# Optimization experiments

Measured on AMD Instinct MI355X. Metric: run time of the kernel, lower is better.

The kernel has to match this reference:

```python
import jax, jax.numpy as jnp
import numpy as np

B, S, H = 1, 2048, 1024
NH, NKV, D = 16, 4, 64
E, TOPK, F = 8, 2, 1024
EPS = 1e-5
ALPHA = 1.702
LIMIT = 7.0
THETA = 10000.0


def setup_inputs() -> dict:
    key = jax.random.key(0)
    ks = jax.random.split(key, 16)
    rn = lambda k, shape, s=0.02: (jax.random.normal(k, shape, jnp.float32) * s)
    qkv_out = (NH + 2 * NKV) * D
    return {
        "hidden_states": jax.random.normal(ks[0], (B, S, H), jnp.float32),
        "residual": jax.random.normal(ks[1], (B, S, H), jnp.float32),
        "positions": jnp.broadcast_to(jnp.arange(S, dtype=jnp.int32), (B, S)),
        "ln1_w": jnp.ones((H,), jnp.float32),
        "ln2_w": jnp.ones((H,), jnp.float32),
        "qkv_w": rn(ks[2], (qkv_out, H)),
        "qkv_b": rn(ks[3], (qkv_out,)),
        "sinks": rn(ks[4], (NH,), 1.0),
        "o_w": rn(ks[5], (H, NH * D)),
        "o_b": rn(ks[6], (H,)),
        "router_w": rn(ks[7], (E, H)),
        "router_b": rn(ks[8], (E,)),
        "gate_up_w": rn(ks[9], (E, 2 * F, H)),
        "gate_up_b": rn(ks[10], (E, 2 * F)),
        "down_w": rn(ks[11], (E, H, F)),
        "down_b": rn(ks[12], (E, H)),
    }


def _rmsnorm(x, w):
    return x * jax.lax.rsqrt(jnp.mean(x * x, -1, keepdims=True) + EPS) * w


def _rope(x, pos):
    # x: [B, S, Hn, D]; pos: [B, S]
    half = D // 2
    inv_freq = 1.0 / (THETA ** (jnp.arange(half, dtype=jnp.float32) / half))
    ang = pos.astype(jnp.float32)[..., None] * inv_freq            # [B,S,half]
    cos = jnp.concatenate([jnp.cos(ang)] * 2, -1)[:, :, None, :]    # [B,S,1,D]
    sin = jnp.concatenate([jnp.sin(ang)] * 2, -1)[:, :, None, :]
    x1, x2 = x[..., :half], x[..., half:]
    rot = jnp.concatenate([-x2, x1], -1)
    return x * cos + rot * sin


def reference(hidden_states, residual, positions, ln1_w, ln2_w, qkv_w, qkv_b,
              sinks, o_w, o_b, router_w, router_b, gate_up_w, gate_up_b,
              down_w, down_b):
    # --- fused RMSNorm + residual (pre-attn) ---
    res1 = hidden_states + residual
    h = _rmsnorm(res1, ln1_w)

    # --- attention ---
    qkv = h @ qkv_w.T + qkv_b
    q, k, v = jnp.split(qkv, [NH * D, NH * D + NKV * D], axis=-1)
    Q = _rope(q.reshape(B, S, NH, D), positions).transpose(0, 2, 1, 3)   # [B,NH,S,D]
    K = _rope(k.reshape(B, S, NKV, D), positions).transpose(0, 2, 1, 3)  # [B,NKV,S,D]
    V = v.reshape(B, S, NKV, D).transpose(0, 2, 1, 3)
    g = NH // NKV
    K = jnp.repeat(K, g, axis=1)
    V = jnp.repeat(V, g, axis=1)
    scores = jnp.einsum('bhqd,bhkd->bhqk', Q, K) * (D ** -0.5)
    causal = jnp.tril(jnp.ones((S, S), bool))
    scores = jnp.where(causal, scores, -1e30)
    sink = jnp.broadcast_to(sinks[None, :, None, None], (B, NH, S, 1))
    probs = jax.nn.softmax(jnp.concatenate([scores, sink], -1), axis=-1)[..., :S]
    attn = jnp.einsum('bhqk,bhkd->bhqd', probs, V)
    attn = attn.transpose(0, 2, 1, 3).reshape(B, S, NH * D)
    attn = attn @ o_w.T + o_b

    # --- fused RMSNorm + residual (post-attn) ---
    res2 = attn + res1
    h2 = _rmsnorm(res2, ln2_w)

    # --- MoE: top-k router + gated expert MLPs ---
    x = h2.reshape(-1, H)                                  # [T,H]
    logits = x @ router_w.T + router_b                      # [T,E]
    vals, idx = jax.lax.top_k(logits, TOPK)
    w = jax.nn.softmax(vals, axis=-1)
    T = B * S
    rscores = jnp.zeros_like(logits).at[jnp.arange(T)[:, None], idx].set(w)  # [T,E]
    gu = jnp.einsum('th,efh->tef', x, gate_up_w) + gate_up_b  # [T,E,2F]
    gate = jnp.minimum(gu[..., 0::2], LIMIT)
    up = jnp.clip(gu[..., 1::2], -LIMIT, LIMIT)
    glu = gate * jax.nn.sigmoid(gate * ALPHA)
    act = (up + 1.0) * glu                                   # [T,E,F]
    eout = jnp.einsum('tef,ehf->teh', act, down_w) + down_b   # [T,E,H]
    moe = jnp.einsum('teh,te->th', eout, rscores).reshape(B, S, H)
    return moe, res2
```

## Files before the change

### kernel.cpp

```cpp
#include <hip/hip_runtime.h>
#include <math.h>

constexpr int S_ = 2048, H_ = 1024, NH_ = 16, NKV_ = 4, D_ = 64;
constexpr int QKV_ = (NH_ + 2 * NKV_) * D_;
constexpr int E_ = 8, F_ = 1024;
constexpr float EPS_ = 1e-5f, ALPHA_ = 1.702f, LIMIT_ = 7.0f;

typedef __attribute__((ext_vector_type(8))) short short8;
typedef __attribute__((ext_vector_type(4))) float f32x4;

__device__ __forceinline__ short f2bf(float f) {
  union { float f; unsigned u; } v; v.f = f;
  unsigned r = v.u + 0x7fffu + ((v.u >> 16) & 1u);
  return (short)(r >> 16);
}

__device__ __forceinline__ void gload_lds16(const void* g, void* l) {
  __builtin_amdgcn_global_load_lds((const __attribute__((address_space(1))) void*)g,
                                   (__attribute__((address_space(3))) void*)l, 16, 0, 0);
}

__global__ __launch_bounds__(256) void k_cvt(const float* __restrict__ in,
                                             short* __restrict__ out, int n4) {
  int i = blockIdx.x * 256 + threadIdx.x;
  int stride = gridDim.x * 256;
  for (; i < n4; i += stride) {
    float4 v = ((const float4*)in)[i];
    short4 o;
    o.x = f2bf(v.x); o.y = f2bf(v.y); o.z = f2bf(v.z); o.w = f2bf(v.w);
    ((short4*)out)[i] = o;
  }
}

__global__ __launch_bounds__(256) void k_norm(const float* __restrict__ x,
                                              const float* __restrict__ add,
                                              const float* __restrict__ w,
                                              float* __restrict__ sum_out,
                                              float* __restrict__ nrm_out,
                                              short* __restrict__ nrm_bf) {
  int t = blockIdx.x, tid = threadIdx.x;
  int lane = tid & 63, wid = tid >> 6;
  float v[4];
  float ss = 0.f;
#pragma unroll
  for (int i = 0; i < 4; i++) {
    int c = i * 256 + tid;
    float a = x[(size_t)t * H_ + c];
    if (add) a += add[(size_t)t * H_ + c];
    v[i] = a;
    ss += a * a;
  }
#pragma unroll
  for (int off = 32; off > 0; off >>= 1) ss += __shfl_xor(ss, off);
  __shared__ float red[4];
  __shared__ float scsh;
  if (lane == 0) red[wid] = ss;
  __syncthreads();
  if (tid == 0) scsh = rsqrtf((red[0] + red[1] + red[2] + red[3]) * (1.f / H_) + EPS_);
  __syncthreads();
  float sc = scsh;
#pragma unroll
  for (int i = 0; i < 4; i++) {
    int c = i * 256 + tid;
    float nv = v[i] * sc * w[c];
    if (sum_out) sum_out[(size_t)t * H_ + c] = v[i];
    if (nrm_out) nrm_out[(size_t)t * H_ + c] = nv;
    if (nrm_bf)  nrm_bf[(size_t)t * H_ + c] = f2bf(nv);
  }
}

__device__ __forceinline__ void mfma_core(const short* __restrict__ A, int lda,
                                          const short* __restrict__ B, int ldb,
                                          int n0, int K,
                                          const int* rows_sh, char* smem,
                                          f32x4 acc[4][4]) {
  const int tid = threadIdx.x;
  const int wid = tid >> 6, lane = tid & 63;
  const int wr = wid >> 1, wc = wid & 1;
  const int fl = lane & 15, fh = lane >> 4;
  const short* src[4];
  unsigned lofs[4];
  {
    const int kofs = (lane & 3) * 8;
    const int r4 = lane >> 2;
#pragma unroll
    for (int j = 0; j < 4; j++) {
      int inst = (wid & 1) * 4 + j;
      int row = inst * 16 + r4;
      if (wid < 2) {
        src[j] = A + (size_t)rows_sh[row] * lda + kofs;
        lofs[j] = inst * 1024u;
      } else {
        src[j] = B + (size_t)(n0 + row) * ldb + kofs;
        lofs[j] = 8192u + inst * 1024u;
      }
    }
  }
  char* As = smem;
  char* Bs = smem + 8192;
  const int abase = (wr * 64 + fl) * 64 + fh * 16;
  const int bbase = (wc * 64 + fl) * 64 + fh * 16;
  for (int kt = 0; kt < K; kt += 32) {
#pragma unroll
    for (int j = 0; j < 4; j++) gload_lds16(src[j] + kt, smem + lofs[j]);
    asm volatile("s_waitcnt vmcnt(0)" ::: "memory");
    __syncthreads();
    short8 a[4], b[4];
#pragma unroll
    for (int mi = 0; mi < 4; mi++) a[mi] = *(const short8*)(As + abase + mi * 1024);
#pragma unroll
    for (int nj = 0; nj < 4; nj++) b[nj] = *(const short8*)(Bs + bbase + nj * 1024);
#pragma unroll
    for (int mi = 0; mi < 4; mi++)
#pragma unroll
      for (int nj = 0; nj < 4; nj++)
        acc[mi][nj] = __builtin_amdgcn_mfma_f32_16x16x32_bf16(a[mi], b[nj], acc[mi][nj], 0, 0, 0);
    __syncthreads();
  }
}

__global__ __launch_bounds__(256) void k_mfma_qkv(const short* __restrict__ A,
                                                  const short* __restrict__ W,
                                                  const float* __restrict__ bias,
                                                  float* __restrict__ out) {
  __shared__ __align__(16) char smem[16384];
  __shared__ int rows_sh[128];
  int m0 = blockIdx.y * 128, n0 = blockIdx.x * 128;
  int tid = threadIdx.x;
  if (tid < 128) rows_sh[tid] = m0 + tid;
  __syncthreads();
  f32x4 acc[4][4] = {};
  mfma_core(A, H_, W, H_, n0, H_, rows_sh, smem, acc);
  const int wid = tid >> 6, lane = tid & 63;
  const int wr = wid >> 1, wc = wid & 1, fl = lane & 15, fh = lane >> 4;
#pragma unroll
  for (int mi = 0; mi < 4; mi++)
#pragma unroll
    for (int nj = 0; nj < 4; nj++) {
      int c = n0 + wc * 64 + nj * 16 + fl;
      float bv = bias[c];
#pragma unroll
      for (int j = 0; j < 4; j++) {
        int r = m0 + wr * 64 + mi * 16 + fh * 4 + j;
        out[(size_t)r * QKV_ + c] = acc[mi][nj][j] + bv;
      }
    }
}

__global__ __launch_bounds__(256) void k_mfma_o(const short* __restrict__ A,
                                                const short* __restrict__ W,
                                                const float* __restrict__ bias,
                                                const float* __restrict__ res1,
                                                float* __restrict__ res2) {
  __shared__ __align__(16) char smem[16384];
  __shared__ int rows_sh[128];
  int m0 = blockIdx.y * 128, n0 = blockIdx.x * 128;
  int tid = threadIdx.x;
  if (tid < 128) rows_sh[tid] = m0 + tid;
  __syncthreads();
  f32x4 acc[4][4] = {};
  mfma_core(A, H_, W, H_, n0, H_, rows_sh, smem, acc);
  const int wid = tid >> 6, lane = tid & 63;
  const int wr = wid >> 1, wc = wid & 1, fl = lane & 15, fh = lane >> 4;
#pragma unroll
  for (int mi = 0; mi < 4; mi++)
#pragma unroll
    for (int nj = 0; nj < 4; nj++) {
      int c = n0 + wc * 64 + nj * 16 + fl;
      float bv = bias[c];
#pragma unroll
      for (int j = 0; j < 4; j++) {
        int r = m0 + wr * 64 + mi * 16 + fh * 4 + j;
        res2[(size_t)r * H_ + c] = acc[mi][nj][j] + bv + res1[(size_t)r * H_ + c];
      }
    }
}

__global__ void k_rope_cvt(const float* __restrict__ qkv, const int* __restrict__ positions,
                           short* __restrict__ qb, short* __restrict__ kb) {
  int idx = blockIdx.x * 256 + threadIdx.x;
  int i = idx & 31;
  int hd = (idx >> 5) % 20;
  int t = idx / (20 * 32);
  const float* base = qkv + (size_t)t * QKV_ + (hd < NH_ ? hd * D_ : NH_ * D_ + (hd - NH_) * D_);
  float pos = (float)positions[t];
  float invf = powf(10000.f, -(float)i * (1.f / 32.f));
  float ang = pos * invf;
  float sn, cs;
  sincosf(ang, &sn, &cs);
  float x1 = base[i], x2 = base[i + 32];
  float r1 = x1 * cs - x2 * sn;
  float r2 = x2 * cs + x1 * sn;
  if (hd < NH_) {
    short* o = qb + (size_t)t * H_ + hd * D_;
    o[i]      = f2bf(r1 * 0.125f);
    o[i + 32] = f2bf(r2 * 0.125f);
  } else {
    short* o = kb + (size_t)t * (NKV_ * D_) + (hd - NH_) * D_;
    o[i]      = f2bf(r1);
    o[i + 32] = f2bf(r2);
  }
}

__global__ __launch_bounds__(256) void k_vcvt(const float* __restrict__ qkv,
                                              short* __restrict__ vbT) {
  int id = blockIdx.x * 256 + threadIdx.x;
  int t = id & (S_ - 1);
  int rest = id >> 11;
  int d = rest & 63;
  int kvh = rest >> 6;
  vbT[id] = f2bf(qkv[(size_t)t * QKV_ + (NH_ + NKV_) * D_ + kvh * D_ + d]);
}

__global__ __launch_bounds__(256) void k_attn_mfma(const short* __restrict__ qb,
                                                   const short* __restrict__ kb,
                                                   const short* __restrict__ vbT,
                                                   const float* __restrict__ sinks,
                                                   short* __restrict__ attnb) {
  const int h = blockIdx.y;
  const int kvh = h >> 2;
  const int tid = threadIdx.x;
  const int wid = tid >> 6, lane = tid & 63;
  const int fl = lane & 15, fh = lane >> 4;

  __shared__ __align__(16) short Ks[64 * 64];
  __shared__ __align__(16) short Vts[64 * 64];
  __shared__ short Pl[4][16][72];

  const float snk = sinks[h];
  const int srcoff = 8 * ((lane & 7) ^ (lane >> 3));
  const int srow = lane >> 3;

#pragma unroll
  for (int rep = 0; rep < 2; rep++) {
    const int qt = rep == 0 ? blockIdx.x : 31 - blockIdx.x;
    const int qbase = qt * 64;
    const int qrow = qbase + wid * 16 + fl;
    short8 qa[2];
#pragma unroll
    for (int p = 0; p < 2; p++)
      qa[p] = *(const short8*)(qb + (size_t)qrow * H_ + h * 64 + p * 32 + fh * 8);

    float mreg[4], lreg[4];
    f32x4 oacc[4] = {};
#pragma unroll
    for (int j = 0; j < 4; j++) { mreg[j] = -1e30f; lreg[j] = 0.f; }

    for (int kc = 0; kc <= qt; kc++) {
#pragma unroll
      for (int ii = 0; ii < 2; ii++) {
        int inst = wid * 2 + ii;
        int krow = kc * 64 + inst * 8 + srow;
        gload_lds16(kb + (size_t)krow * (NKV_ * D_) + kvh * D_ + srcoff,
                    (char*)Ks + inst * 1024);
        int drow = inst * 8 + srow;
        gload_lds16(vbT + (size_t)(kvh * 64 + drow) * S_ + kc * 64 + srcoff,
                    (char*)Vts + inst * 1024);
      }
      asm volatile("s_waitcnt vmcnt(0)" ::: "memory");
      __syncthreads();

      f32x4 sacc[4] = {};
#pragma unroll
      for (int p = 0; p < 2; p++) {
        const int cswz_base = (p * 4 + fh);
#pragma unroll
        for (int t = 0; t < 4; t++) {
          int r = t * 16 + fl;
          short8 kf = *(const short8*)((const char*)Ks + r * 128 + 16 * (cswz_base ^ (fl & 7)));
          sacc[t] = __builtin_amdgcn_mfma_f32_16x16x32_bf16(qa[p], kf, sacc[t], 0, 0, 0);
        }
      }
      if (kc == qt) {
#pragma unroll
        for (int t = 0; t < 4; t++) {
          int key = kc * 64 + t * 16 + fl;
#pragma unroll
          for (int j = 0; j < 4; j++) {
            int q = qbase + wid * 16 + fh * 4 + j;
            if (key > q) sacc[t][j] = -1e30f;
          }
        }
      }
#pragma unroll
      for (int j = 0; j < 4; j++) {
        float vm = fmaxf(fmaxf(sacc[0][j], sacc[1][j]), fmaxf(sacc[2][j], sacc[3][j]));
        vm = fmaxf(vm, __shfl_xor(vm, 1));
        vm = fmaxf(vm, __shfl_xor(vm, 2));
        vm = fmaxf(vm, __shfl_xor(vm, 4));
        vm = fmaxf(vm, __shfl_xor(vm, 8));
        float mn = fmaxf(mreg[j], vm);
        float sf = __expf(mreg[j] - mn);
        float ps = 0.f;
#pragma unroll
        for (int t = 0; t < 4; t++) {
          float pv = __expf(sacc[t][j] - mn);
          ps += pv;
          Pl[wid][fh * 4 + j][t * 16 + fl] = f2bf(pv);
        }
        ps += __shfl_xor(ps, 1);
        ps += __shfl_xor(ps, 2);
        ps += __shfl_xor(ps, 4);
        ps += __shfl_xor(ps, 8);
        lreg[j] = lreg[j] * sf + ps;
        mreg[j] = mn;
#pragma unroll
        for (int u = 0; u < 4; u++) oacc[u][j] *= sf;
      }
#pragma unroll
      for (int p = 0; p < 2; p++) {
        short8 pa = *(const short8*)((const char*)&Pl[wid][0][0] + fl * 144 + p * 64 + fh * 16);
        const int cswz_base = (p * 4 + fh);
#pragma unroll
        for (int u = 0; u < 4; u++) {
          int r = u * 16 + fl;
          short8 vf = *(const short8*)((const char*)Vts + r * 128 + 16 * (cswz_base ^ (fl & 7)));
          oacc[u] = __builtin_amdgcn_mfma_f32_16x16x32_bf16(pa, vf, oacc[u], 0, 0, 0);
        }
      }
      __syncthreads();
    }
#pragma unroll
    for (int j = 0; j < 4; j++) {
      float mf = fmaxf(mreg[j], snk);
      float denom = lreg[j] * __expf(mreg[j] - mf) + __expf(snk - mf);
      float osc = __expf(mreg[j] - mf) / denom;
      int q = qbase + wid * 16 + fh * 4 + j;
#pragma unroll
      for (int u = 0; u < 4; u++)
        attnb[(size_t)q * H_ + h * 64 + u * 16 + fl] = f2bf(oacc[u][j] * osc);
    }
  }
}

__global__ __launch_bounds__(64) void k_router(const float* __restrict__ h2,
                                               const float* __restrict__ rw,
                                               const float* __restrict__ rb,
                                               int* __restrict__ counts,
                                               int* __restrict__ perm,
                                               float* __restrict__ pw) {
  int t = blockIdx.x, lane = threadIdx.x;
  float acc[E_];
#pragma unroll
  for (int e = 0; e < E_; e++) acc[e] = 0.f;
  for (int i = 0; i < 16; i++) {
    float x = h2[(size_t)t * H_ + i * 64 + lane];
#pragma unroll
    for (int e = 0; e < E_; e++) acc[e] += x * rw[e * H_ + i * 64 + lane];
  }
#pragma unroll
  for (int e = 0; e < E_; e++) {
#pragma unroll
    for (int off = 32; off > 0; off >>= 1) acc[e] += __shfl_xor(acc[e], off);
  }
  if (lane == 0) {
    float lg[E_];
#pragma unroll
    for (int e = 0; e < E_; e++) lg[e] = acc[e] + rb[e];
    int i0 = 0;
    float v0 = lg[0];
    for (int e = 1; e < E_; e++)
      if (lg[e] > v0) { v0 = lg[e]; i0 = e; }
    int i1 = -1;
    float v1 = -INFINITY;
    for (int e = 0; e < E_; e++) {
      if (e == i0) continue;
      if (lg[e] > v1) { v1 = lg[e]; i1 = e; }
    }
    float ex = expf(v1 - v0);
    float w0 = 1.f / (1.f + ex);
    float w1 = ex * w0;
    int p0 = atomicAdd(&counts[i0], 1);
    if (p0 < S_) { perm[i0 * S_ + p0] = t * 2;     pw[i0 * S_ + p0] = w0; }
    int p1 = atomicAdd(&counts[i1], 1);
    if (p1 < S_) { perm[i1 * S_ + p1] = t * 2 + 1; pw[i1 * S_ + p1] = w1; }
  }
}

__global__ __launch_bounds__(256) void k_mfma_gu(const short* __restrict__ h2b,
                                                 const short* __restrict__ W,
                                                 const float* __restrict__ gu_b,
                                                 const int* __restrict__ counts,
                                                 const int* __restrict__ perm,
                                                 short* __restrict__ actb) {
  int e = blockIdx.z;
  int cnt = counts[e];
  if (cnt < 0) cnt = 0;
  if (cnt > S_) cnt = S_;
  int m0 = blockIdx.y * 128;
  if (m0 >= cnt) return;
  int n0 = blockIdx.x * 128;
  __shared__ __align__(16) char smem[16384];
  __shared__ int rows_sh[128];
  __shared__ int slots_sh[128];
  int tid = threadIdx.x;
  if (tid < 128) {
    int idx = m0 + tid;
    int p = (idx < cnt) ? perm[e * S_ + idx] : -1;
    if (p < 0 || p >= 2 * S_) p = -1;
    slots_sh[tid] = p;
    rows_sh[tid] = (p >= 0) ? (p >> 1) : 0;
  }
  __syncthreads();
  f32x4 acc[4][4] = {};
  mfma_core(h2b, H_, W + (size_t)e * 2 * F_ * H_, H_, n0, H_, rows_sh, smem, acc);
  const int wid = tid >> 6, lane = tid & 63;
  const int wr = wid >> 1, wc = wid & 1, fl = lane & 15, fh = lane >> 4;
  const float* gub = gu_b + (size_t)e * 2 * F_;
#pragma unroll
  for (int mi = 0; mi < 4; mi++)
#pragma unroll
    for (int nj = 0; nj < 4; nj++) {
      int c = n0 + wc * 64 + nj * 16 + fl;
      float bv = gub[c];
#pragma unroll
      for (int j = 0; j < 4; j++) {
        int r = wr * 64 + mi * 16 + fh * 4 + j;
        float v = acc[mi][nj][j] + bv;
        float other = __shfl_xor(v, 1);
        if (!(lane & 1)) {
          int slot = slots_sh[r];
          if (slot >= 0) {
            float g = fminf(v, LIMIT_);
            float u = fminf(fmaxf(other, -LIMIT_), LIMIT_);
            float a = (u + 1.f) * (g / (1.f + expf(-g * ALPHA_)));
            actb[(size_t)slot * F_ + (c >> 1)] = f2bf(a);
          }
        }
      }
    }
}

__global__ __launch_bounds__(256) void k_mfma_down(const short* __restrict__ actb,
                                                   const short* __restrict__ W,
                                                   const float* __restrict__ dn_b,
                                                   const int* __restrict__ counts,
                                                   const int* __restrict__ perm,
                                                   const float* __restrict__ pw,
                                                   float* __restrict__ dnout) {
  int e = blockIdx.z;
  int cnt = counts[e];
  if (cnt < 0) cnt = 0;
  if (cnt > S_) cnt = S_;
  int m0 = blockIdx.y * 128;
  if (m0 >= cnt) return;
  int n0 = blockIdx.x * 128;
  __shared__ __align__(16) char smem[16384];
  __shared__ int rows_sh[128];
  __shared__ float wts_sh[128];
  int tid = threadIdx.x;
  if (tid < 128) {
    int idx = m0 + tid;
    int p = 0;
    float w = 0.f;
    if (idx < cnt) { p = perm[e * S_ + idx]; w = pw[e * S_ + idx]; }
    if (p < 0 || p >= 2 * S_) { p = 0; w = 0.f; }
    rows_sh[tid] = p;
    wts_sh[tid] = w;
  }
  __syncthreads();
  f32x4 acc[4][4] = {};
  mfma_core(actb, F_, rows_sh == nullptr ? actb : (W + (size_t)e * H_ * F_), F_, n0, F_, rows_sh, smem, acc);
  const int wid = tid >> 6, lane = tid & 63;
  const int wr = wid >> 1, wc = wid & 1, fl = lane & 15, fh = lane >> 4;
  const float* dnb = dn_b + (size_t)e * H_;
#pragma unroll
  for (int mi = 0; mi < 4; mi++)
#pragma unroll
    for (int nj = 0; nj < 4; nj++) {
      int c = n0 + wc * 64 + nj * 16 + fl;
      float bv = dnb[c];
#pragma unroll
      for (int j = 0; j < 4; j++) {
        int r = wr * 64 + mi * 16 + fh * 4 + j;
        if (m0 + r < cnt) {
          int slot = rows_sh[r];
          dnout[(size_t)slot * H_ + c] = (acc[mi][nj][j] + bv) * wts_sh[r];
        }
      }
    }
}

__global__ __launch_bounds__(256) void k_combine(const float* __restrict__ dnout,
                                                 float* __restrict__ out) {
  int i = blockIdx.x * 256 + threadIdx.x;
  int t = i >> 8, c = i & 255;
  const float4* a = (const float4*)dnout;
  float4 x = a[(size_t)(2 * t) * 256 + c];
  float4 y = a[(size_t)(2 * t + 1) * 256 + c];
  float4 o;
  o.x = x.x + y.x; o.y = x.y + y.y; o.z = x.z + y.z; o.w = x.w + y.w;
  ((float4*)out)[i] = o;
}

extern "C" void kernel_launch(void* const* d_in, const int* in_sizes, int n_in,
                              void* d_out, int out_size, void* d_ws, size_t ws_size,
                              hipStream_t stream) {
  (void)in_sizes; (void)n_in; (void)out_size; (void)ws_size;
  const float* hidden   = (const float*)d_in[0];
  const float* residual = (const float*)d_in[1];
  const int*   positions= (const int*)d_in[2];
  const float* ln1_w    = (const float*)d_in[3];
  const float* ln2_w    = (const float*)d_in[4];
  const float* qkv_w    = (const float*)d_in[5];
  const float* qkv_b    = (const float*)d_in[6];
  const float* sinks    = (const float*)d_in[7];
  const float* o_w      = (const float*)d_in[8];
  const float* o_b      = (const float*)d_in[9];
  const float* router_w = (const float*)d_in[10];
  const float* router_b = (const float*)d_in[11];
  const float* gu_w     = (const float*)d_in[12];
  const float* gu_b     = (const float*)d_in[13];
  const float* dn_w     = (const float*)d_in[14];
  const float* dn_b     = (const float*)d_in[15];

  float* out_moe = (float*)d_out;
  float* res2 = (float*)d_out + (size_t)S_ * H_;

  char* ws = (char*)d_ws;
  size_t off = 0;
  auto alloc = [&](size_t bytes) {
    void* p = ws + off;
    off = (off + bytes + 255) & ~(size_t)255;
    return p;
  };
  int*   counts  = (int*)alloc(E_ * sizeof(int));
  int*   perm    = (int*)alloc((size_t)E_ * S_ * sizeof(int));
  float* pw      = (float*)alloc((size_t)E_ * S_ * sizeof(float));
  float* res1    = (float*)alloc((size_t)S_ * H_ * 4);
  short* hbuf_b  = (short*)alloc((size_t)S_ * H_ * 2);
  float* qkv     = (float*)alloc((size_t)S_ * QKV_ * 4);
  short* qb      = (short*)alloc((size_t)S_ * H_ * 2);
  short* kb      = (short*)alloc((size_t)S_ * NKV_ * D_ * 2);
  short* vbT     = (short*)alloc((size_t)S_ * NKV_ * D_ * 2);
  short* attnb   = (short*)alloc((size_t)S_ * H_ * 2);
  float* h2      = (float*)alloc((size_t)S_ * H_ * 4);
  short* h2b     = (short*)alloc((size_t)S_ * H_ * 2);
  short* actb    = (short*)alloc((size_t)2 * S_ * F_ * 2);
  float* dnout   = (float*)alloc((size_t)2 * S_ * H_ * 4);
  short* qkv_wb  = (short*)alloc((size_t)QKV_ * H_ * 2);
  short* o_wb    = (short*)alloc((size_t)H_ * H_ * 2);
  short* gu_wb   = (short*)alloc((size_t)E_ * 2 * F_ * H_ * 2);
  short* dn_wb   = (short*)alloc((size_t)E_ * H_ * F_ * 2);

  hipMemsetAsync(counts, 0, E_ * sizeof(int), stream);

  k_cvt<<<1024, 256, 0, stream>>>(qkv_w, qkv_wb, QKV_ * H_ / 4);
  k_cvt<<<1024, 256, 0, stream>>>(o_w, o_wb, H_ * H_ / 4);
  k_cvt<<<2048, 256, 0, stream>>>(gu_w, gu_wb, E_ * 2 * F_ * H_ / 4);
  k_cvt<<<2048, 256, 0, stream>>>(dn_w, dn_wb, E_ * H_ * F_ / 4);

  k_norm<<<S_, 256, 0, stream>>>(hidden, residual, ln1_w, res1, nullptr, hbuf_b);
  k_mfma_qkv<<<dim3(QKV_ / 128, S_ / 128), 256, 0, stream>>>(hbuf_b, qkv_wb, qkv_b, qkv);
  k_rope_cvt<<<(S_ * 20 * 32) / 256, 256, 0, stream>>>(qkv, positions, qb, kb);
  k_vcvt<<<(S_ * NKV_ * D_) / 256, 256, 0, stream>>>(qkv, vbT);
  k_attn_mfma<<<dim3(16, NH_), 256, 0, stream>>>(qb, kb, vbT, sinks, attnb);
  k_mfma_o<<<dim3(H_ / 128, S_ / 128), 256, 0, stream>>>(attnb, o_wb, o_b, res1, res2);
  k_norm<<<S_, 256, 0, stream>>>(res2, nullptr, ln2_w, nullptr, h2, h2b);
  k_router<<<S_, 64, 0, stream>>>(h2, router_w, router_b, counts, perm, pw);
  k_mfma_gu<<<dim3(2 * F_ / 128, S_ / 128, E_), 256, 0, stream>>>(h2b, gu_wb, gu_b, counts, perm, actb);
  k_mfma_down<<<dim3(H_ / 128, S_ / 128, E_), 256, 0, stream>>>(actb, dn_wb, dn_b, counts, perm, pw, dnout);
  k_combine<<<(S_ * H_ / 4) / 256, 256, 0, stream>>>(dnout, out_moe);
}
```

Measured before the change: 451.3 us.

## Double-buffer GEMM and attention loads, fuse router into norm, atomic MoE combine

```diff
diff --git a/kernel.cpp b/kernel.cpp
--- a/kernel.cpp
+++ b/kernel.cpp
@@ -36,8 +36,12 @@
                                               const float* __restrict__ add,
                                               const float* __restrict__ w,
                                               float* __restrict__ sum_out,
-                                              float* __restrict__ nrm_out,
-                                              short* __restrict__ nrm_bf) {
+                                              short* __restrict__ nrm_bf,
+                                              const float* __restrict__ rw,
+                                              const float* __restrict__ rb,
+                                              int* __restrict__ counts,
+                                              int* __restrict__ perm,
+                                              float* __restrict__ pw) {
   int t = blockIdx.x, tid = threadIdx.x;
   int lane = tid & 63, wid = tid >> 6;
   float v[4];
@@ -59,13 +63,58 @@
   if (tid == 0) scsh = rsqrtf((red[0] + red[1] + red[2] + red[3]) * (1.f / H_) + EPS_);
   __syncthreads();
   float sc = scsh;
+  float nv[4];
 #pragma unroll
   for (int i = 0; i < 4; i++) {
     int c = i * 256 + tid;
-    float nv = v[i] * sc * w[c];
+    nv[i] = v[i] * sc * w[c];
     if (sum_out) sum_out[(size_t)t * H_ + c] = v[i];
-    if (nrm_out) nrm_out[(size_t)t * H_ + c] = nv;
-    if (nrm_bf)  nrm_bf[(size_t)t * H_ + c] = f2bf(nv);
+    nrm_bf[(size_t)t * H_ + c] = f2bf(nv[i]);
+  }
+  if (rw) {
+    float acc[E_];
+#pragma unroll
+    for (int e = 0; e < E_; e++) acc[e] = 0.f;
+#pragma unroll
+    for (int i = 0; i < 4; i++) {
+      int c = i * 256 + tid;
+#pragma unroll
+      for (int e = 0; e < E_; e++) acc[e] += nv[i] * rw[e * H_ + c];
+    }
+#pragma unroll
+    for (int e = 0; e < E_; e++) {
+#pragma unroll
+      for (int off = 32; off > 0; off >>= 1) acc[e] += __shfl_xor(acc[e], off);
+    }
+    __shared__ float rsh[4][E_];
+    if (lane == 0) {
+#pragma unroll
+      for (int e = 0; e < E_; e++) rsh[wid][e] = acc[e];
+    }
+    __syncthreads();
+    if (tid == 0) {
+      float lg[E_];
+#pragma unroll
+      for (int e = 0; e < E_; e++)
+        lg[e] = rsh[0][e] + rsh[1][e] + rsh[2][e] + rsh[3][e] + rb[e];
+      int i0 = 0;
+      float v0 = lg[0];
+      for (int e = 1; e < E_; e++)
+        if (lg[e] > v0) { v0 = lg[e]; i0 = e; }
+      int i1 = -1;
+      float v1 = -INFINITY;
+      for (int e = 0; e < E_; e++) {
+        if (e == i0) continue;
+        if (lg[e] > v1) { v1 = lg[e]; i1 = e; }
+      }
+      float ex = __expf(v1 - v0);
+      float w0 = 1.f / (1.f + ex);
+      float w1 = ex * w0;
+      int p0 = atomicAdd(&counts[i0], 1);
+      if (p0 < S_) { perm[i0 * S_ + p0] = t * 2;     pw[i0 * S_ + p0] = w0; }
+      int p1 = atomicAdd(&counts[i1], 1);
+      if (p1 < S_) { perm[i1 * S_ + p1] = t * 2 + 1; pw[i1 * S_ + p1] = w1; }
+    }
   }
 }
 
@@ -96,15 +145,25 @@
       }
     }
   }
-  char* As = smem;
-  char* Bs = smem + 8192;
   const int abase = (wr * 64 + fl) * 64 + fh * 16;
   const int bbase = (wc * 64 + fl) * 64 + fh * 16;
-  for (int kt = 0; kt < K; kt += 32) {
-#pragma unroll
-    for (int j = 0; j < 4; j++) gload_lds16(src[j] + kt, smem + lofs[j]);
-    asm volatile("s_waitcnt vmcnt(0)" ::: "memory");
+  const int T = K >> 5;
+#pragma unroll
+  for (int j = 0; j < 4; j++) gload_lds16(src[j], smem + lofs[j]);
+  int cur = 0;
+  for (int t = 0; t < T; t++) {
+    if (t + 1 < T) {
+      int kt = (t + 1) << 5;
+#pragma unroll
+      for (int j = 0; j < 4; j++)
+        gload_lds16(src[j] + kt, smem + ((cur ^ 1) * 16384u + lofs[j]));
+      asm volatile("s_waitcnt vmcnt(4)" ::: "memory");
+    } else {
+      asm volatile("s_waitcnt vmcnt(0)" ::: "memory");
+    }
     __syncthreads();
+    const char* As = smem + cur * 16384u;
+    const char* Bs = As + 8192;
     short8 a[4], b[4];
 #pragma unroll
     for (int mi = 0; mi < 4; mi++) a[mi] = *(const short8*)(As + abase + mi * 1024);
@@ -116,6 +175,7 @@
       for (int nj = 0; nj < 4; nj++)
         acc[mi][nj] = __builtin_amdgcn_mfma_f32_16x16x32_bf16(a[mi], b[nj], acc[mi][nj], 0, 0, 0);
     __syncthreads();
+    cur ^= 1;
   }
 }
 
@@ -123,7 +183,7 @@
                                                   const short* __restrict__ W,
                                                   const float* __restrict__ bias,
                                                   float* __restrict__ out) {
-  __shared__ __align__(16) char smem[16384];
+  __shared__ __align__(16) char smem[32768];
   __shared__ int rows_sh[128];
   int m0 = blockIdx.y * 128, n0 = blockIdx.x * 128;
   int tid = threadIdx.x;
@@ -152,7 +212,7 @@
                                                 const float* __restrict__ bias,
                                                 const float* __restrict__ res1,
                                                 float* __restrict__ res2) {
-  __shared__ __align__(16) char smem[16384];
+  __shared__ __align__(16) char smem[32768];
   __shared__ int rows_sh[128];
   int m0 = blockIdx.y * 128, n0 = blockIdx.x * 128;
   int tid = threadIdx.x;
@@ -184,10 +244,9 @@
   int t = idx / (20 * 32);
   const float* base = qkv + (size_t)t * QKV_ + (hd < NH_ ? hd * D_ : NH_ * D_ + (hd - NH_) * D_);
   float pos = (float)positions[t];
-  float invf = powf(10000.f, -(float)i * (1.f / 32.f));
+  float invf = exp2f(-(float)i * 0.4152410118609203f);
   float ang = pos * invf;
-  float sn, cs;
-  sincosf(ang, &sn, &cs);
+  float sn = __sinf(ang), cs = __cosf(ang);
   float x1 = base[i], x2 = base[i + 32];
   float r1 = x1 * cs - x2 * sn;
   float r2 = x2 * cs + x1 * sn;
@@ -202,14 +261,24 @@
   }
 }
 
-__global__ __launch_bounds__(256) void k_vcvt(const float* __restrict__ qkv,
-                                              short* __restrict__ vbT) {
-  int id = blockIdx.x * 256 + threadIdx.x;
-  int t = id & (S_ - 1);
-  int rest = id >> 11;
-  int d = rest & 63;
-  int kvh = rest >> 6;
-  vbT[id] = f2bf(qkv[(size_t)t * QKV_ + (NH_ + NKV_) * D_ + kvh * D_ + d]);
+__global__ __launch_bounds__(256) void k_vtrans(const float* __restrict__ qkv,
+                                                short* __restrict__ vbT) {
+  __shared__ short tile[64][65];
+  int t0 = blockIdx.x * 64;
+  int kvh = blockIdx.y;
+  int tid = threadIdx.x;
+  int r = tid >> 6, c = tid & 63;
+#pragma unroll
+  for (int i = 0; i < 16; i++) {
+    int row = i * 4 + r;
+    tile[row][c] = f2bf(qkv[(size_t)(t0 + row) * QKV_ + (NH_ + NKV_) * D_ + kvh * D_ + c]);
+  }
+  __syncthreads();
+#pragma unroll
+  for (int i = 0; i < 16; i++) {
+    int d = i * 4 + r;
+    vbT[(size_t)(kvh * 64 + d) * S_ + t0 + c] = tile[c][d];
+  }
 }
 
 __global__ __launch_bounds__(256) void k_attn_mfma(const short* __restrict__ qb,
@@ -219,161 +288,127 @@
                                                    short* __restrict__ attnb) {
   const int h = blockIdx.y;
   const int kvh = h >> 2;
+  const int qt = (h < 8) ? blockIdx.x : 31 - blockIdx.x;
   const int tid = threadIdx.x;
   const int wid = tid >> 6, lane = tid & 63;
   const int fl = lane & 15, fh = lane >> 4;
 
-  __shared__ __align__(16) short Ks[64 * 64];
-  __shared__ __align__(16) short Vts[64 * 64];
+  __shared__ __align__(16) short Ks[2][4096];
+  __shared__ __align__(16) short Vts[2][4096];
   __shared__ short Pl[4][16][72];
 
   const float snk = sinks[h];
   const int srcoff = 8 * ((lane & 7) ^ (lane >> 3));
   const int srow = lane >> 3;
 
-#pragma unroll
-  for (int rep = 0; rep < 2; rep++) {
-    const int qt = rep == 0 ? blockIdx.x : 31 - blockIdx.x;
-    const int qbase = qt * 64;
-    const int qrow = qbase + wid * 16 + fl;
-    short8 qa[2];
-#pragma unroll
-    for (int p = 0; p < 2; p++)
-      qa[p] = *(const short8*)(qb + (size_t)qrow * H_ + h * 64 + p * 32 + fh * 8);
-
-    float mreg[4], lreg[4];
-    f32x4 oacc[4] = {};
-#pragma unroll
-    for (int j = 0; j < 4; j++) { mreg[j] = -1e30f; lreg[j] = 0.f; }
-
-    for (int kc = 0; kc <= qt; kc++) {
+  const int qbase = qt * 64;
+  const int qrow = qbase + wid * 16 + fl;
+  short8 qa[2];
+#pragma unroll
+  for (int p = 0; p < 2; p++)
+    qa[p] = *(const short8*)(qb + (size_t)qrow * H_ + h * 64 + p * 32 + fh * 8);
+
+  float mreg[4], lreg[4];
+  f32x4 oacc[4] = {};
+#pragma unroll
+  for (int j = 0; j < 4; j++) { mreg[j] = -1e30f; lreg[j] = 0.f; }
+
+#pragma unroll
+  for (int ii = 0; ii < 2; ii++) {
+    int inst = wid * 2 + ii;
+    gload_lds16(kb + (size_t)(inst * 8 + srow) * (NKV_ * D_) + kvh * D_ + srcoff,
+                (char*)Ks[0] + inst * 1024);
+    gload_lds16(vbT + (size_t)(kvh * 64 + inst * 8 + srow) * S_ + srcoff,
+                (char*)Vts[0] + inst * 1024);
+  }
+  int cur = 0;
+  for (int kc = 0; kc <= qt; kc++) {
+    if (kc < qt) {
+      int kn = kc + 1;
 #pragma unroll
       for (int ii = 0; ii < 2; ii++) {
         int inst = wid * 2 + ii;
-        int krow = kc * 64 + inst * 8 + srow;
-        gload_lds16(kb + (size_t)krow * (NKV_ * D_) + kvh * D_ + srcoff,
-                    (char*)Ks + inst * 1024);
-        int drow = inst * 8 + srow;
-        gload_lds16(vbT + (size_t)(kvh * 64 + drow) * S_ + kc * 64 + srcoff,
-                    (char*)Vts + inst * 1024);
-      }
+        gload_lds16(kb + (size_t)(kn * 64 + inst * 8 + srow) * (NKV_ * D_) + kvh * D_ + srcoff,
+                    (char*)Ks[cur ^ 1] + inst * 1024);
+        gload_lds16(vbT + (size_t)(kvh * 64 + inst * 8 + srow) * S_ + kn * 64 + srcoff,
+                    (char*)Vts[cur ^ 1] + inst * 1024);
+      }
+      asm volatile("s_waitcnt vmcnt(4)" ::: "memory");
+    } else {
       asm volatile("s_waitcnt vmcnt(0)" ::: "memory");
-      __syncthreads();
-
-      f32x4 sacc[4] = {};
-#pragma unroll
-      for (int p = 0; p < 2; p++) {
-        const int cswz_base = (p * 4 + fh);
-#pragma unroll
-        for (int t = 0; t < 4; t++) {
-          int r = t * 16 + fl;
-          short8 kf = *(const short8*)((const char*)Ks + r * 128 + 16 * (cswz_base ^ (fl & 7)));
-          sacc[t] = __builtin_amdgcn_mfma_f32_16x16x32_bf16(qa[p], kf, sacc[t], 0, 0, 0);
+    }
+    __syncthreads();
+
+    f32x4 sacc[4] = {};
+#pragma unroll
+    for (int p = 0; p < 2; p++) {
+      const int cswz_base = (p * 4 + fh);
+#pragma unroll
+      for (int t = 0; t < 4; t++) {
+        int r = t * 16 + fl;
+        short8 kf = *(const short8*)((const char*)Ks[cur] + r * 128 + 16 * (cswz_base ^ (fl & 7)));
+        sacc[t] = __builtin_amdgcn_mfma_f32_16x16x32_bf16(qa[p], kf, sacc[t], 0, 0, 0);
+      }
+    }
+    if (kc == qt) {
+#pragma unroll
+      for (int t = 0; t < 4; t++) {
+        int key = kc * 64 + t * 16 + fl;
+#pragma unroll
+        for (int j = 0; j < 4; j++) {
+          int q = qbase + wid * 16 + fh * 4 + j;
+          if (key > q) sacc[t][j] = -1e30f;
         }
       }
-      if (kc == qt) {
-#pragma unroll
-        for (int t = 0; t < 4; t++) {
-          int key = kc * 64 + t * 16 + fl;
-#pragma unroll
-          for (int j = 0; j < 4; j++) {
-            int q = qbase + wid * 16 + fh * 4 + j;
-            if (key > q) sacc[t][j] = -1e30f;
-          }
-        }
-      }
-#pragma unroll
-      for (int j = 0; j < 4; j++) {
-        float vm = fmaxf(fmaxf(sacc[0][j], sacc[1][j]), fmaxf(sacc[2][j], sacc[3][j]));
-        vm = fmaxf(vm, __shfl_xor(vm, 1));
-        vm = fmaxf(vm, __shfl_xor(vm, 2));
-        vm = fmaxf(vm, __shfl_xor(vm, 4));
-        vm = fmaxf(vm, __shfl_xor(vm, 8));
-        float mn = fmaxf(mreg[j], vm);
-        float sf = __expf(mreg[j] - mn);
-        float ps = 0.f;
-#pragma unroll
-        for (int t = 0; t < 4; t++) {
-          float pv = __expf(sacc[t][j] - mn);
-          ps += pv;
-          Pl[wid][fh * 4 + j][t * 16 + fl] = f2bf(pv);
-        }
-        ps += __shfl_xor(ps, 1);
-        ps += __shfl_xor(ps, 2);
-        ps += __shfl_xor(ps, 4);
-        ps += __shfl_xor(ps, 8);
-        lreg[j] = lreg[j] * sf + ps;
-        mreg[j] = mn;
-#pragma unroll
-        for (int u = 0; u < 4; u++) oacc[u][j] *= sf;
-      }
-#pragma unroll
-      for (int p = 0; p < 2; p++) {
-        short8 pa = *(const short8*)((const char*)&Pl[wid][0][0] + fl * 144 + p * 64 + fh * 16);
-        const int cswz_base = (p * 4 + fh);
-#pragma unroll
-        for (int u = 0; u < 4; u++) {
-          int r = u * 16 + fl;
-          short8 vf = *(const short8*)((const char*)Vts + r * 128 + 16 * (cswz_base ^ (fl & 7)));
-          oacc[u] = __builtin_amdgcn_mfma_f32_16x16x32_bf16(pa, vf, oacc[u], 0, 0, 0);
-        }
-      }
-      __syncthreads();
     }
 #pragma unroll
     for (int j = 0; j < 4; j++) {
-      float mf = fmaxf(mreg[j], snk);
-      float denom = lreg[j] * __expf(mreg[j] - mf) + __expf(snk - mf);
-      float osc = __expf(mreg[j] - mf) / denom;
-      int q = qbase + wid * 16 + fh * 4 + j;
-#pragma unroll
-      for (int u = 0; u < 4; u++)
-        attnb[(size_t)q * H_ + h * 64 + u * 16 + fl] = f2bf(oacc[u][j] * osc);
-    }
-  }
-}
-
-__global__ __launch_bounds__(64) void k_router(const float* __restrict__ h2,
-                                               const float* __restrict__ rw,
-                                               const float* __restrict__ rb,
-                                               int* __restrict__ counts,
-                                               int* __restrict__ perm,
-                                               float* __restrict__ pw) {
-  int t = blockIdx.x, lane = threadIdx.x;
-  float acc[E_];
-#pragma unroll
-  for (int e = 0; e < E_; e++) acc[e] = 0.f;
-  for (int i = 0; i < 16; i++) {
-    float x = h2[(size_t)t * H_ + i * 64 + lane];
-#pragma unroll
-    for (int e = 0; e < E_; e++) acc[e] += x * rw[e * H_ + i * 64 + lane];
-  }
-#pragma unroll
-  for (int e = 0; e < E_; e++) {
-#pragma unroll
-    for (int off = 32; off > 0; off >>= 1) acc[e] += __shfl_xor(acc[e], off);
-  }
-  if (lane == 0) {
-    float lg[E_];
-#pragma unroll
-    for (int e = 0; e < E_; e++) lg[e] = acc[e] + rb[e];
-    int i0 = 0;
-    float v0 = lg[0];
-    for (int e = 1; e < E_; e++)
-      if (lg[e] > v0) { v0 = lg[e]; i0 = e; }
-    int i1 = -1;
-    float v1 = -INFINITY;
-    for (int e = 0; e < E_; e++) {
-      if (e == i0) continue;
-      if (lg[e] > v1) { v1 = lg[e]; i1 = e; }
-    }
-    float ex = expf(v1 - v0);
-    float w0 = 1.f / (1.f + ex);
-    float w1 = ex * w0;
-    int p0 = atomicAdd(&counts[i0], 1);
-    if (p0 < S_) { perm[i0 * S_ + p0] = t * 2;     pw[i0 * S_ + p0] = w0; }
-    int p1 = atomicAdd(&counts[i1], 1);
-    if (p1 < S_) { perm[i1 * S_ + p1] = t * 2 + 1; pw[i1 * S_ + p1] = w1; }
+      float vm = fmaxf(fmaxf(sacc[0][j], sacc[1][j]), fmaxf(sacc[2][j], sacc[3][j]));
+      vm = fmaxf(vm, __shfl_xor(vm, 1));
+      vm = fmaxf(vm, __shfl_xor(vm, 2));
+      vm = fmaxf(vm, __shfl_xor(vm, 4));
+      vm = fmaxf(vm, __shfl_xor(vm, 8));
+      float mn = fmaxf(mreg[j], vm);
+      float sf = __expf(mreg[j] - mn);
+      float ps = 0.f;
+#pragma unroll
+      for (int t = 0; t < 4; t++) {
+        float pv = __expf(sacc[t][j] - mn);
+        ps += pv;
+        Pl[wid][fh * 4 + j][t * 16 + fl] = f2bf(pv);
+      }
+      ps += __shfl_xor(ps, 1);
+      ps += __shfl_xor(ps, 2);
+      ps += __shfl_xor(ps, 4);
+      ps += __shfl_xor(ps, 8);
+      lreg[j] = lreg[j] * sf + ps;
+      mreg[j] = mn;
+#pragma unroll
+      for (int u = 0; u < 4; u++) oacc[u][j] *= sf;
+    }
+#pragma unroll
+    for (int p = 0; p < 2; p++) {
+      short8 pa = *(const short8*)((const char*)&Pl[wid][0][0] + fl * 144 + p * 64 + fh * 16);
+      const int cswz_base = (p * 4 + fh);
+#pragma unroll
+      for (int u = 0; u < 4; u++) {
+        int r = u * 16 + fl;
+        short8 vf = *(const short8*)((const char*)Vts[cur] + r * 128 + 16 * (cswz_base ^ (fl & 7)));
+        oacc[u] = __builtin_amdgcn_mfma_f32_16x16x32_bf16(pa, vf, oacc[u], 0, 0, 0);
+      }
+    }
+    __syncthreads();
+    cur ^= 1;
+  }
+#pragma unroll
+  for (int j = 0; j < 4; j++) {
+    float mf = fmaxf(mreg[j], snk);
+    float denom = lreg[j] * __expf(mreg[j] - mf) + __expf(snk - mf);
+    float osc = __expf(mreg[j] - mf) / denom;
+    int q = qbase + wid * 16 + fh * 4 + j;
+#pragma unroll
+    for (int u = 0; u < 4; u++)
+      attnb[(size_t)q * H_ + h * 64 + u * 16 + fl] = f2bf(oacc[u][j] * osc);
   }
 }
 
@@ -390,7 +425,7 @@
   int m0 = blockIdx.y * 128;
   if (m0 >= cnt) return;
   int n0 = blockIdx.x * 128;
-  __shared__ __align__(16) char smem[16384];
+  __shared__ __align__(16) char smem[32768];
   __shared__ int rows_sh[128];
   __shared__ int slots_sh[128];
   int tid = threadIdx.x;
@@ -423,7 +458,7 @@
           if (slot >= 0) {
             float g = fminf(v, LIMIT_);
             float u = fminf(fmaxf(other, -LIMIT_), LIMIT_);
-            float a = (u + 1.f) * (g / (1.f + expf(-g * ALPHA_)));
+            float a = (u + 1.f) * (g / (1.f + __expf(-g * ALPHA_)));
             actb[(size_t)slot * F_ + (c >> 1)] = f2bf(a);
           }
         }
@@ -437,7 +472,7 @@
                                                    const int* __restrict__ counts,
                                                    const int* __restrict__ perm,
                                                    const float* __restrict__ pw,
-                                                   float* __restrict__ dnout) {
+                                                   float* __restrict__ out_moe) {
   int e = blockIdx.z;
   int cnt = counts[e];
   if (cnt < 0) cnt = 0;
@@ -445,7 +480,7 @@
   int m0 = blockIdx.y * 128;
   if (m0 >= cnt) return;
   int n0 = blockIdx.x * 128;
-  __shared__ __align__(16) char smem[16384];
+  __shared__ __align__(16) char smem[32768];
   __shared__ int rows_sh[128];
   __shared__ float wts_sh[128];
   int tid = threadIdx.x;
@@ -460,7 +495,7 @@
   }
   __syncthreads();
   f32x4 acc[4][4] = {};
-  mfma_core(actb, F_, rows_sh == nullptr ? actb : (W + (size_t)e * H_ * F_), F_, n0, F_, rows_sh, smem, acc);
+  mfma_core(actb, F_, W + (size_t)e * H_ * F_, F_, n0, F_, rows_sh, smem, acc);
   const int wid = tid >> 6, lane = tid & 63;
   const int wr = wid >> 1, wc = wid & 1, fl = lane & 15, fh = lane >> 4;
   const float* dnb = dn_b + (size_t)e * H_;
@@ -475,22 +510,11 @@
         int r = wr * 64 + mi * 16 + fh * 4 + j;
         if (m0 + r < cnt) {
           int slot = rows_sh[r];
-          dnout[(size_t)slot * H_ + c] = (acc[mi][nj][j] + bv) * wts_sh[r];
+          float val = (acc[mi][nj][j] + bv) * wts_sh[r];
+          atomicAdd(&out_moe[(size_t)(slot >> 1) * H_ + c], val);
         }
       }
     }
-}
-
-__global__ __launch_bounds__(256) void k_combine(const float* __restrict__ dnout,
-                                                 float* __restrict__ out) {
-  int i = blockIdx.x * 256 + threadIdx.x;
-  int t = i >> 8, c = i & 255;
-  const float4* a = (const float4*)dnout;
-  float4 x = a[(size_t)(2 * t) * 256 + c];
-  float4 y = a[(size_t)(2 * t + 1) * 256 + c];
-  float4 o;
-  o.x = x.x + y.x; o.y = x.y + y.y; o.z = x.z + y.z; o.w = x.w + y.w;
-  ((float4*)out)[i] = o;
 }
 
 extern "C" void kernel_launch(void* const* d_in, const int* in_sizes, int n_in,
@@ -534,31 +558,30 @@
   short* kb      = (short*)alloc((size_t)S_ * NKV_ * D_ * 2);
   short* vbT     = (short*)alloc((size_t)S_ * NKV_ * D_ * 2);
   short* attnb   = (short*)alloc((size_t)S_ * H_ * 2);
-  float* h2      = (float*)alloc((size_t)S_ * H_ * 4);
   short* h2b     = (short*)alloc((size_t)S_ * H_ * 2);
   short* actb    = (short*)alloc((size_t)2 * S_ * F_ * 2);
-  float* dnout   = (float*)alloc((size_t)2 * S_ * H_ * 4);
   short* qkv_wb  = (short*)alloc((size_t)QKV_ * H_ * 2);
   short* o_wb    = (short*)alloc((size_t)H_ * H_ * 2);
   short* gu_wb   = (short*)alloc((size_t)E_ * 2 * F_ * H_ * 2);
   short* dn_wb   = (short*)alloc((size_t)E_ * H_ * F_ * 2);
 
   hipMemsetAsync(counts, 0, E_ * sizeof(int), stream);
+  hipMemsetAsync(out_moe, 0, (size_t)S_ * H_ * 4, stream);
 
   k_cvt<<<1024, 256, 0, stream>>>(qkv_w, qkv_wb, QKV_ * H_ / 4);
   k_cvt<<<1024, 256, 0, stream>>>(o_w, o_wb, H_ * H_ / 4);
   k_cvt<<<2048, 256, 0, stream>>>(gu_w, gu_wb, E_ * 2 * F_ * H_ / 4);
   k_cvt<<<2048, 256, 0, stream>>>(dn_w, dn_wb, E_ * H_ * F_ / 4);
 
-  k_norm<<<S_, 256, 0, stream>>>(hidden, residual, ln1_w, res1, nullptr, hbuf_b);
+  k_norm<<<S_, 256, 0, stream>>>(hidden, residual, ln1_w, res1, hbuf_b,
+                                 nullptr, nullptr, nullptr, nullptr, nullptr);
   k_mfma_qkv<<<dim3(QKV_ / 128, S_ / 128), 256, 0, stream>>>(hbuf_b, qkv_wb, qkv_b, qkv);
   k_rope_cvt<<<(S_ * 20 * 32) / 256, 256, 0, stream>>>(qkv, positions, qb, kb);
-  k_vcvt<<<(S_ * NKV_ * D_) / 256, 256, 0, stream>>>(qkv, vbT);
-  k_attn_mfma<<<dim3(16, NH_), 256, 0, stream>>>(qb, kb, vbT, sinks, attnb);
+  k_vtrans<<<dim3(S_ / 64, NKV_), 256, 0, stream>>>(qkv, vbT);
+  k_attn_mfma<<<dim3(32, NH_), 256, 0, stream>>>(qb, kb, vbT, sinks, attnb);
   k_mfma_o<<<dim3(H_ / 128, S_ / 128), 256, 0, stream>>>(attnb, o_wb, o_b, res1, res2);
-  k_norm<<<S_, 256, 0, stream>>>(res2, nullptr, ln2_w, nullptr, h2, h2b);
-  k_router<<<S_, 64, 0, stream>>>(h2, router_w, router_b, counts, perm, pw);
+  k_norm<<<S_, 256, 0, stream>>>(res2, nullptr, ln2_w, nullptr, h2b,
+                                 router_w, router_b, counts, perm, pw);
   k_mfma_gu<<<dim3(2 * F_ / 128, S_ / 128, E_), 256, 0, stream>>>(h2b, gu_wb, gu_b, counts, perm, actb);
-  k_mfma_down<<<dim3(H_ / 128, S_ / 128, E_), 256, 0, stream>>>(actb, dn_wb, dn_b, counts, perm, pw, dnout);
-  k_combine<<<(S_ * H_ / 4) / 256, 256, 0, stream>>>(dnout, out_moe);
-}
+  k_mfma_down<<<dim3(H_ / 128, S_ / 128, E_), 256, 0, stream>>>(actb, dn_wb, dn_b, counts, perm, pw, out_moe);
+}
```

Result: no change. 457.5 us (+1.4%).
